# Performance work log

Measured on AMD Instinct MI355X. Metric: run time of the kernel, lower is better.

The kernel has to match this reference:

```python
import jax, jax.numpy as jnp
import numpy as np

P_THRESH = 20  # p=0.2 * 100
# direction -> (di, dj): masked pixel (i,j) writes input[i,j] to x[i+di, j+dj], then avg to x[i,j]
OFFSETS = {0: (-1, -1), 1: (-1, 0), 2: (-1, 1), 3: (0, -1), 4: (0, 0), 5: (0, 1), 6: (1, -1), 7: (1, 0)}


def _shift(a, di, dj):
    """out[i+di, j+dj] = a[i, j] on last two axes; out-of-range -> 0/False."""
    H, W = a.shape[-2], a.shape[-1]
    pad = [(0, 0)] * (a.ndim - 2) + [(max(di, 0), max(-di, 0)), (max(dj, 0), max(-dj, 0))]
    p = jnp.pad(a, pad)
    sh, sw = max(-di, 0), max(-dj, 0)
    return p[..., sh:sh + H, sw:sw + W]


def _avg3x3_reflect(x):
    H, W = x.shape[-2], x.shape[-1]
    p = jnp.pad(x, [(0, 0), (0, 0), (1, 1), (1, 1)], mode='reflect')
    s = jnp.zeros_like(x)
    for i in range(3):
        for j in range(3):
            s = s + p[..., i:i + H, j:j + W]
    return s / 9.0


def brown_forward(input, dir, prob):
    avg = _avg3x3_reflect(input)
    pos = prob <= P_THRESH
    x = input
    for d in range(8):  # sequential, matching torch in-place write order
        di, dj = OFFSETS[d]
        m = (dir == d) & pos
        if d == 4:
            x = jnp.where(m, avg, x)  # mm: only avg write
        else:
            sm = _shift(m, di, dj)                       # neighbor-target mask
            x = jnp.where(sm, _shift(input, di, dj), x)  # x[i+di,j+dj] = input[i,j]
            mv = _shift(sm, -di, -dj)                    # mask restricted to valid region
            x = jnp.where(mv, avg, x)                    # x[i,j] = avg[i,j]
    return x


def setup_inputs() -> dict:
    key = jax.random.key(0)
    k1, k2, k3 = jax.random.split(key, 3)
    shape = (32, 64, 128, 128)
    return {
        'input': jax.random.normal(k1, shape, dtype=jnp.float32),
        'dir': jax.random.randint(k2, shape, 0, 8, dtype=jnp.int32),
        'prob': jax.random.randint(k3, shape, 1, 100, dtype=jnp.int32),
    }


def reference(input, dir, prob):
    return brown_forward(input, dir, prob)
```

## Files before the change

### kernel.cpp

```cpp
#include <hip/hip_runtime.h>
#include <cstddef>

#define H 128
#define W 128
#define P_THRESH 20

typedef float f4u __attribute__((ext_vector_type(4), aligned(4)));
typedef int   i4u __attribute__((ext_vector_type(4), aligned(4)));
typedef float nf2 __attribute__((ext_vector_type(2)));

__global__ __launch_bounds__(256, 8)
void brown_kernel(const float* __restrict__ inp,
                  const int*  __restrict__ dirp,
                  const int*  __restrict__ prb,
                  float* __restrict__ out)
{
    __shared__ unsigned int s_mk[331];

    const int tid   = threadIdx.x;
    const int bid   = blockIdx.x;
    const int slice = bid >> 4;
    const int r0    = (bid & 15) << 3;
    const size_t base = (size_t)slice * (size_t)(H * W);

    const int lane = tid & 63;
    const int wid  = tid >> 6;
    const int pr   = r0 + (wid << 1);
    const int j0   = lane << 1;

    const int cl  = (lane == 0) ? 0 : ((lane == 63) ? (W - 4) : (j0 - 1));
    const int gA  = (pr == 0) ? 1 : (pr - 1);
    const int gD  = (pr == H - 2) ? (H - 2) : (pr + 2);
    const float* ip = inp + base;
    const f4u iA = *(const f4u*)(ip + (size_t)gA * W + cl);
    const f4u iB = *(const f4u*)(ip + (size_t)pr * W + cl);
    const f4u iC = *(const f4u*)(ip + (size_t)(pr + 1) * W + cl);
    const f4u iD = *(const f4u*)(ip + (size_t)gD * W + cl);

    #pragma unroll
    for (int it = 0; it < 2; ++it) {
        const int idx = it * 256 + tid;
        if (idx < 320) {
            const int lr = idx >> 5;
            const int w  = idx & 31;
            const int gr = r0 + lr - 1;
            unsigned m;
            if ((unsigned)gr < (unsigned)H) {
                const i4u dv = *(const i4u*)(dirp + base + (size_t)gr * W + 4 * w);
                const i4u pv = *(const i4u*)(prb  + base + (size_t)gr * W + 4 * w);
                const unsigned a = (pv.x <= P_THRESH) ? (unsigned)dv.x : 8u;
                const unsigned b = (pv.y <= P_THRESH) ? (unsigned)dv.y : 8u;
                const unsigned c = (pv.z <= P_THRESH) ? (unsigned)dv.z : 8u;
                const unsigned e = (pv.w <= P_THRESH) ? (unsigned)dv.w : 8u;
                m = a | (b << 8) | (c << 16) | (e << 24);
                if (gr == 0) {
                    unsigned mm = 0;
                    #pragma unroll
                    for (int i2 = 0; i2 < 4; ++i2) {
                        unsigned bb = (m >> (8 * i2)) & 255u;
                        bb = (bb <= 2u) ? 8u : bb;
                        mm |= bb << (8 * i2);
                    }
                    m = mm;
                } else if (gr == H - 1) {
                    unsigned mm = 0;
                    #pragma unroll
                    for (int i2 = 0; i2 < 4; ++i2) {
                        unsigned bb = (m >> (8 * i2)) & 255u;
                        bb = (bb >= 6u) ? 8u : bb;
                        mm |= bb << (8 * i2);
                    }
                    m = mm;
                }
                if (w == 0) {
                    const unsigned b0 = m & 255u;
                    if ((0x49u >> b0) & 1u) m = (m & ~255u) | 8u;
                }
                if (w == 31) {
                    const unsigned b3 = m >> 24;
                    if ((0x24u >> b3) & 1u) m = (m & 0x00FFFFFFu) | (8u << 24);
                }
            } else {
                m = 0x08080808u;
            }
            s_mk[1 + 33 * lr + w] = m;
            if (w == 31) s_mk[1 + 33 * lr + 32] = 0x08080808u;
        }
    }
    if (tid == 0) s_mk[0] = 0x08080808u;
    __syncthreads();

    unsigned mr[4];
    #pragma unroll
    for (int dr = 0; dr < 4; ++dr) {
        const int lr   = (wid << 1) + dr;
        const int addr = 132 * lr + (j0 + 3);
        const unsigned w0 = s_mk[addr >> 2];
        const unsigned w1 = s_mk[(addr >> 2) + 1];
        const int sh = 8 * (addr & 3);
        mr[dr] = (w0 >> sh) | (w1 << (32 - sh));
    }

    const bool e0 = (lane == 0), e63 = (lane == 63), eE = e0 | e63;
    auto fixrow = [&](f4u i, float v[4]) {
        v[0] = eE ? i.y : i.x;
        v[1] = e0 ? i.x : (e63 ? i.z : i.y);
        v[2] = e0 ? i.y : (e63 ? i.w : i.z);
        v[3] = eE ? i.z : i.w;
    };
    float v0[4], v1[4], v2[4], v3[4];
    fixrow(iA, v0); fixrow(iB, v1); fixrow(iC, v2); fixrow(iD, v3);

    float s12[4], csT[4], csB[4];
    #pragma unroll
    for (int w = 0; w < 4; ++w) {
        s12[w] = v1[w] + v2[w];
        csT[w] = v0[w] + s12[w];
        csB[w] = s12[w] + v3[w];
    }

    auto crow = [&](unsigned mT, unsigned mM, unsigned mB,
                    const float vT[4], const float vM[4], const float vBo[4],
                    const float cs[4]) -> nf2 {
        nf2 res;
        #pragma unroll
        for (int p = 0; p < 2; ++p) {
            const float avg = (cs[p] + cs[p + 1] + cs[p + 2]) * (1.0f / 9.0f);
            const unsigned wT = mT >> (8 * p);
            const unsigned wM = mM >> (8 * p);
            const unsigned wB = mB >> (8 * p);

            float val = vM[p + 1];
            int dl = -1;
            if (((wB >> 16) & 255u) == 0u) { val = vBo[p + 2]; dl = 0; }
            if (((wB >>  8) & 255u) == 1u) { val = vBo[p + 1]; dl = 1; }
            if (( wB        & 255u) == 2u) { val = vBo[p];     dl = 2; }
            if (((wM >> 16) & 255u) == 3u) { val = vM[p + 2];  dl = 3; }
            if (( wM        & 255u) == 5u) { val = vM[p];      dl = 5; }
            if (((wT >> 16) & 255u) == 6u) { val = vT[p + 2];  dl = 6; }
            if (((wT >>  8) & 255u) == 7u) { val = vT[p + 1];  dl = 7; }

            const int msel = (int)((wM >> 8) & 255u);
            if ((msel < 8) & (msel >= dl)) val = avg;
            res[p] = val;
        }
        return res;
    };

    const nf2 resT = crow(mr[0], mr[1], mr[2], v0, v1, v2, csT);
    const nf2 resB = crow(mr[1], mr[2], mr[3], v1, v2, v3, csB);
    *(nf2*)(out + base + (size_t)pr * W + j0)       = resT;
    *(nf2*)(out + base + (size_t)(pr + 1) * W + j0) = resB;
}

extern "C" void kernel_launch(void* const* d_in, const int* in_sizes, int n_in,
                              void* d_out, int out_size, void* d_ws, size_t ws_size,
                              hipStream_t stream) {
    const float* inp  = (const float*)d_in[0];
    const int*   dirp = (const int*)d_in[1];
    const int*   prb  = (const int*)d_in[2];
    float* out = (float*)d_out;

    const int slices = in_sizes[0] / (H * W);
    const int grid = slices * 16;
    brown_kernel<<<grid, 256, 0, stream>>>(inp, dirp, prb, out);
}
```

Baseline: 383.0 us.

## Retile blocks to process four rows across two slices per block

```diff
diff --git a/kernel.cpp b/kernel.cpp
--- a/kernel.cpp
+++ b/kernel.cpp
@@ -15,39 +15,44 @@
                   const int*  __restrict__ prb,
                   float* __restrict__ out)
 {
-    __shared__ unsigned int s_mk[331];
+    __shared__ unsigned int s_mk[2 * 199];
 
     const int tid   = threadIdx.x;
     const int bid   = blockIdx.x;
-    const int slice = bid >> 4;
-    const int r0    = (bid & 15) << 3;
-    const size_t base = (size_t)slice * (size_t)(H * W);
+    const int spair = bid >> 5;
+    const int r0    = (bid & 31) << 2;
+    const size_t base0 = (size_t)(2 * spair) * (size_t)(H * W);
+    const size_t base1 = base0 + (size_t)(H * W);
 
     const int lane = tid & 63;
-    const int wid  = tid >> 6;
-    const int pr   = r0 + (wid << 1);
+    const int row  = tid >> 6;
+    const int gi   = r0 + row;
     const int j0   = lane << 1;
 
-    const int cl  = (lane == 0) ? 0 : ((lane == 63) ? (W - 4) : (j0 - 1));
-    const int gA  = (pr == 0) ? 1 : (pr - 1);
-    const int gD  = (pr == H - 2) ? (H - 2) : (pr + 2);
-    const float* ip = inp + base;
-    const f4u iA = *(const f4u*)(ip + (size_t)gA * W + cl);
-    const f4u iB = *(const f4u*)(ip + (size_t)pr * W + cl);
-    const f4u iC = *(const f4u*)(ip + (size_t)(pr + 1) * W + cl);
-    const f4u iD = *(const f4u*)(ip + (size_t)gD * W + cl);
+    const int cl = (lane == 0) ? 0 : ((lane == 63) ? (W - 4) : (j0 - 1));
+    const int rT = (gi == 0) ? 1 : gi - 1;
+    const int rB = (gi == H - 1) ? H - 2 : gi + 1;
+    const f4u iT0 = *(const f4u*)(inp + base0 + (size_t)rT * W + cl);
+    const f4u iM0 = *(const f4u*)(inp + base0 + (size_t)gi * W + cl);
+    const f4u iB0 = *(const f4u*)(inp + base0 + (size_t)rB * W + cl);
+    const f4u iT1 = *(const f4u*)(inp + base1 + (size_t)rT * W + cl);
+    const f4u iM1 = *(const f4u*)(inp + base1 + (size_t)gi * W + cl);
+    const f4u iB1 = *(const f4u*)(inp + base1 + (size_t)rB * W + cl);
 
     #pragma unroll
     for (int it = 0; it < 2; ++it) {
         const int idx = it * 256 + tid;
-        if (idx < 320) {
-            const int lr = idx >> 5;
-            const int w  = idx & 31;
-            const int gr = r0 + lr - 1;
+        if (idx < 384) {
+            const int s  = (idx >= 192);
+            const int k  = idx - s * 192;
+            const int r6 = k >> 5;
+            const int w  = k & 31;
+            const int gr = r0 + r6 - 1;
+            const size_t bs = s ? base1 : base0;
             unsigned m;
             if ((unsigned)gr < (unsigned)H) {
-                const i4u dv = *(const i4u*)(dirp + base + (size_t)gr * W + 4 * w);
-                const i4u pv = *(const i4u*)(prb  + base + (size_t)gr * W + 4 * w);
+                const i4u dv = *(const i4u*)(dirp + bs + (size_t)gr * W + 4 * w);
+                const i4u pv = *(const i4u*)(prb  + bs + (size_t)gr * W + 4 * w);
                 const unsigned a = (pv.x <= P_THRESH) ? (unsigned)dv.x : 8u;
                 const unsigned b = (pv.y <= P_THRESH) ? (unsigned)dv.y : 8u;
                 const unsigned c = (pv.z <= P_THRESH) ? (unsigned)dv.z : 8u;
@@ -83,23 +88,12 @@
             } else {
                 m = 0x08080808u;
             }
-            s_mk[1 + 33 * lr + w] = m;
-            if (w == 31) s_mk[1 + 33 * lr + 32] = 0x08080808u;
+            s_mk[s * 199 + 1 + 33 * r6 + w] = m;
+            if (w == 31) s_mk[s * 199 + 1 + 33 * r6 + 32] = 0x08080808u;
         }
     }
-    if (tid == 0) s_mk[0] = 0x08080808u;
+    if (tid < 2) s_mk[tid * 199] = 0x08080808u;
     __syncthreads();
-
-    unsigned mr[4];
-    #pragma unroll
-    for (int dr = 0; dr < 4; ++dr) {
-        const int lr   = (wid << 1) + dr;
-        const int addr = 132 * lr + (j0 + 3);
-        const unsigned w0 = s_mk[addr >> 2];
-        const unsigned w1 = s_mk[(addr >> 2) + 1];
-        const int sh = 8 * (addr & 3);
-        mr[dr] = (w0 >> sh) | (w1 << (32 - sh));
-    }
 
     const bool e0 = (lane == 0), e63 = (lane == 63), eE = e0 | e63;
     auto fixrow = [&](f4u i, float v[4]) {
@@ -108,20 +102,18 @@
         v[2] = e0 ? i.y : (e63 ? i.w : i.z);
         v[3] = eE ? i.z : i.w;
     };
-    float v0[4], v1[4], v2[4], v3[4];
-    fixrow(iA, v0); fixrow(iB, v1); fixrow(iC, v2); fixrow(iD, v3);
-
-    float s12[4], csT[4], csB[4];
-    #pragma unroll
-    for (int w = 0; w < 4; ++w) {
-        s12[w] = v1[w] + v2[w];
-        csT[w] = v0[w] + s12[w];
-        csB[w] = s12[w] + v3[w];
-    }
-
+    auto mwin = [&](int s, int dr) -> unsigned {
+        const int addr = 132 * (row + dr) + (j0 + 3);
+        const unsigned w0 = s_mk[s * 199 + (addr >> 2)];
+        const unsigned w1 = s_mk[s * 199 + (addr >> 2) + 1];
+        const int sh = 8 * (addr & 3);
+        return (w0 >> sh) | (w1 << (32 - sh));
+    };
     auto crow = [&](unsigned mT, unsigned mM, unsigned mB,
-                    const float vT[4], const float vM[4], const float vBo[4],
-                    const float cs[4]) -> nf2 {
+                    const float vT[4], const float vM[4], const float vBo[4]) -> nf2 {
+        float cs[4];
+        #pragma unroll
+        for (int w = 0; w < 4; ++w) cs[w] = vT[w] + vM[w] + vBo[w];
         nf2 res;
         #pragma unroll
         for (int p = 0; p < 2; ++p) {
@@ -147,10 +139,18 @@
         return res;
     };
 
-    const nf2 resT = crow(mr[0], mr[1], mr[2], v0, v1, v2, csT);
-    const nf2 resB = crow(mr[1], mr[2], mr[3], v1, v2, v3, csB);
-    *(nf2*)(out + base + (size_t)pr * W + j0)       = resT;
-    *(nf2*)(out + base + (size_t)(pr + 1) * W + j0) = resB;
+    {
+        float vT[4], vM[4], vB[4];
+        fixrow(iT0, vT); fixrow(iM0, vM); fixrow(iB0, vB);
+        const nf2 r = crow(mwin(0, 0), mwin(0, 1), mwin(0, 2), vT, vM, vB);
+        *(nf2*)(out + base0 + (size_t)gi * W + j0) = r;
+    }
+    {
+        float vT[4], vM[4], vB[4];
+        fixrow(iT1, vT); fixrow(iM1, vM); fixrow(iB1, vB);
+        const nf2 r = crow(mwin(1, 0), mwin(1, 1), mwin(1, 2), vT, vM, vB);
+        *(nf2*)(out + base1 + (size_t)gi * W + j0) = r;
+    }
 }
 
 extern "C" void kernel_launch(void* const* d_in, const int* in_sizes, int n_in,
@@ -162,6 +162,6 @@
     float* out = (float*)d_out;
 
     const int slices = in_sizes[0] / (H * W);
-    const int grid = slices * 16;
+    const int grid = (slices >> 1) * 32;
     brown_kernel<<<grid, 256, 0, stream>>>(inp, dirp, prb, out);
 }
```

Measured after the change: 384.4 us. About the same (+0.4%).

## Replace shared-memory mask staging with per-wave loads and cross-lane shuffles

Applied to the files above, without the earlier changes.

```diff
diff --git a/kernel.cpp b/kernel.cpp
--- a/kernel.cpp
+++ b/kernel.cpp
@@ -9,14 +9,12 @@
 typedef int   i4u __attribute__((ext_vector_type(4), aligned(4)));
 typedef float nf2 __attribute__((ext_vector_type(2)));
 
-__global__ __launch_bounds__(256, 8)
+__global__ __launch_bounds__(256, 6)
 void brown_kernel(const float* __restrict__ inp,
                   const int*  __restrict__ dirp,
                   const int*  __restrict__ prb,
                   float* __restrict__ out)
 {
-    __shared__ unsigned int s_mk[331];
-
     const int tid   = threadIdx.x;
     const int bid   = blockIdx.x;
     const int slice = bid >> 4;
@@ -24,82 +22,87 @@
     const size_t base = (size_t)slice * (size_t)(H * W);
 
     const int lane = tid & 63;
-    const int wid  = tid >> 6;
-    const int pr   = r0 + (wid << 1);
+    const int wv   = tid >> 6;
+    const int pr   = r0 + (wv << 1);
     const int j0   = lane << 1;
+    const int w    = lane & 31;
+    const bool hi  = lane >= 32;
 
-    const int cl  = (lane == 0) ? 0 : ((lane == 63) ? (W - 4) : (j0 - 1));
-    const int gA  = (pr == 0) ? 1 : (pr - 1);
-    const int gD  = (pr == H - 2) ? (H - 2) : (pr + 2);
+    const int cl = (lane == 0) ? 0 : ((lane == 63) ? (W - 4) : (j0 - 1));
+    const int gA = (pr == 0) ? 1 : pr - 1;
+    const int gD = (pr == 126) ? 126 : pr + 2;
     const float* ip = inp + base;
     const f4u iA = *(const f4u*)(ip + (size_t)gA * W + cl);
     const f4u iB = *(const f4u*)(ip + (size_t)pr * W + cl);
     const f4u iC = *(const f4u*)(ip + (size_t)(pr + 1) * W + cl);
     const f4u iD = *(const f4u*)(ip + (size_t)gD * W + cl);
 
-    #pragma unroll
-    for (int it = 0; it < 2; ++it) {
-        const int idx = it * 256 + tid;
-        if (idx < 320) {
-            const int lr = idx >> 5;
-            const int w  = idx & 31;
-            const int gr = r0 + lr - 1;
-            unsigned m;
-            if ((unsigned)gr < (unsigned)H) {
-                const i4u dv = *(const i4u*)(dirp + base + (size_t)gr * W + 4 * w);
-                const i4u pv = *(const i4u*)(prb  + base + (size_t)gr * W + 4 * w);
-                const unsigned a = (pv.x <= P_THRESH) ? (unsigned)dv.x : 8u;
-                const unsigned b = (pv.y <= P_THRESH) ? (unsigned)dv.y : 8u;
-                const unsigned c = (pv.z <= P_THRESH) ? (unsigned)dv.z : 8u;
-                const unsigned e = (pv.w <= P_THRESH) ? (unsigned)dv.w : 8u;
-                m = a | (b << 8) | (c << 16) | (e << 24);
-                if (gr == 0) {
-                    unsigned mm = 0;
-                    #pragma unroll
-                    for (int i2 = 0; i2 < 4; ++i2) {
-                        unsigned bb = (m >> (8 * i2)) & 255u;
-                        bb = (bb <= 2u) ? 8u : bb;
-                        mm |= bb << (8 * i2);
-                    }
-                    m = mm;
-                } else if (gr == H - 1) {
-                    unsigned mm = 0;
-                    #pragma unroll
-                    for (int i2 = 0; i2 < 4; ++i2) {
-                        unsigned bb = (m >> (8 * i2)) & 255u;
-                        bb = (bb >= 6u) ? 8u : bb;
-                        mm |= bb << (8 * i2);
-                    }
-                    m = mm;
-                }
-                if (w == 0) {
-                    const unsigned b0 = m & 255u;
-                    if ((0x49u >> b0) & 1u) m = (m & ~255u) | 8u;
-                }
-                if (w == 31) {
-                    const unsigned b3 = m >> 24;
-                    if ((0x24u >> b3) & 1u) m = (m & 0x00FFFFFFu) | (8u << 24);
-                }
-            } else {
-                m = 0x08080808u;
-            }
-            s_mk[1 + 33 * lr + w] = m;
-            if (w == 31) s_mk[1 + 33 * lr + 32] = 0x08080808u;
+    const int grA_ = hi ? pr : pr - 1;
+    const int grB_ = hi ? pr + 2 : pr + 1;
+    const int grA = (grA_ < 0) ? 0 : grA_;
+    const int grB = (grB_ > H - 1) ? H - 1 : grB_;
+    const i4u dvA = *(const i4u*)(dirp + base + (size_t)grA * W + 4 * w);
+    const i4u pvA = *(const i4u*)(prb  + base + (size_t)grA * W + 4 * w);
+    const i4u dvB = *(const i4u*)(dirp + base + (size_t)grB * W + 4 * w);
+    const i4u pvB = *(const i4u*)(prb  + base + (size_t)grB * W + 4 * w);
+
+    auto packm = [](i4u d, i4u p) -> unsigned {
+        const unsigned a = (p.x <= P_THRESH) ? (unsigned)d.x : 8u;
+        const unsigned b = (p.y <= P_THRESH) ? (unsigned)d.y : 8u;
+        const unsigned c = (p.z <= P_THRESH) ? (unsigned)d.z : 8u;
+        const unsigned e = (p.w <= P_THRESH) ? (unsigned)d.w : 8u;
+        return a | (b << 8) | (c << 16) | (e << 24);
+    };
+    unsigned rA = packm(dvA, pvA);
+    unsigned rB = packm(dvB, pvB);
+
+    if (w == 0) {
+        const unsigned bA = rA & 255u;
+        if ((0x49u >> bA) & 1u) rA = (rA & ~255u) | 8u;
+        const unsigned bB = rB & 255u;
+        if ((0x49u >> bB) & 1u) rB = (rB & ~255u) | 8u;
+    }
+    if (w == 31) {
+        const unsigned bA = rA >> 24;
+        if ((0x24u >> bA) & 1u) rA = (rA & 0x00FFFFFFu) | (8u << 24);
+        const unsigned bB = rB >> 24;
+        if ((0x24u >> bB) & 1u) rB = (rB & 0x00FFFFFFu) | (8u << 24);
+    }
+    if (pr == 0) {
+        unsigned f = 0;
+        #pragma unroll
+        for (int i2 = 0; i2 < 4; ++i2) {
+            unsigned bb = (rA >> (8 * i2)) & 255u;
+            bb = (bb <= 2u) ? 8u : bb;
+            f |= bb << (8 * i2);
         }
+        rA = hi ? f : 0x08080808u;
+    } else if (pr == 126) {
+        unsigned f = 0;
+        #pragma unroll
+        for (int i2 = 0; i2 < 4; ++i2) {
+            unsigned bb = (rB >> (8 * i2)) & 255u;
+            bb = (bb >= 6u) ? 8u : bb;
+            f |= bb << (8 * i2);
+        }
+        rB = hi ? 0x08080808u : f;
     }
-    if (tid == 0) s_mk[0] = 0x08080808u;
-    __syncthreads();
 
-    unsigned mr[4];
-    #pragma unroll
-    for (int dr = 0; dr < 4; ++dr) {
-        const int lr   = (wid << 1) + dr;
-        const int addr = 132 * lr + (j0 + 3);
-        const unsigned w0 = s_mk[addr >> 2];
-        const unsigned w1 = s_mk[(addr >> 2) + 1];
-        const int sh = 8 * (addr & 3);
-        mr[dr] = (w0 >> sh) | (w1 << (32 - sh));
-    }
+    const int w0 = (lane == 0)  ? 0  : ((j0 - 1) >> 2);
+    const int w1 = (lane == 63) ? 31 : ((j0 + 2) >> 2);
+    const int sh = (lane & 1) ? 8 : 24;
+    auto mwin = [&](unsigned regv, int sel) -> unsigned {
+        const unsigned s0 = __shfl(regv, sel + w0, 64);
+        const unsigned s1 = __shfl(regv, sel + w1, 64);
+        unsigned win = (s0 >> sh) | (s1 << (32 - sh));
+        if (lane == 0)  win = (s0 << 8) | 8u;
+        if (lane == 63) win = (s0 >> 8) | 0x08000000u;
+        return win;
+    };
+    const unsigned mT = mwin(rA, 0);
+    const unsigned mM = mwin(rA, 32);
+    const unsigned mC = mwin(rB, 0);
+    const unsigned mB2 = mwin(rB, 32);
 
     const bool e0 = (lane == 0), e63 = (lane == 63), eE = e0 | e63;
     auto fixrow = [&](f4u i, float v[4]) {
@@ -113,22 +116,22 @@
 
     float s12[4], csT[4], csB[4];
     #pragma unroll
-    for (int w = 0; w < 4; ++w) {
-        s12[w] = v1[w] + v2[w];
-        csT[w] = v0[w] + s12[w];
-        csB[w] = s12[w] + v3[w];
+    for (int k = 0; k < 4; ++k) {
+        s12[k] = v1[k] + v2[k];
+        csT[k] = v0[k] + s12[k];
+        csB[k] = s12[k] + v3[k];
     }
 
-    auto crow = [&](unsigned mT, unsigned mM, unsigned mB,
+    auto crow = [&](unsigned mTa, unsigned mMa, unsigned mBa,
                     const float vT[4], const float vM[4], const float vBo[4],
                     const float cs[4]) -> nf2 {
         nf2 res;
         #pragma unroll
         for (int p = 0; p < 2; ++p) {
             const float avg = (cs[p] + cs[p + 1] + cs[p + 2]) * (1.0f / 9.0f);
-            const unsigned wT = mT >> (8 * p);
-            const unsigned wM = mM >> (8 * p);
-            const unsigned wB = mB >> (8 * p);
+            const unsigned wT = mTa >> (8 * p);
+            const unsigned wM = mMa >> (8 * p);
+            const unsigned wB = mBa >> (8 * p);
 
             float val = vM[p + 1];
             int dl = -1;
@@ -147,8 +150,8 @@
         return res;
     };
 
-    const nf2 resT = crow(mr[0], mr[1], mr[2], v0, v1, v2, csT);
-    const nf2 resB = crow(mr[1], mr[2], mr[3], v1, v2, v3, csB);
+    const nf2 resT = crow(mT, mM, mC,  v0, v1, v2, csT);
+    const nf2 resB = crow(mM, mC, mB2, v1, v2, v3, csB);
     *(nf2*)(out + base + (size_t)pr * W + j0)       = resT;
     *(nf2*)(out + base + (size_t)(pr + 1) * W + j0) = resB;
 }
```

Measured after the change: 380.6 us. About the same (-0.6%).
